# Kernel tuning notes

Hardware: AMD Instinct MI355X
Metric: run time of the kernel (lower is better)

## Reference

```python
import jax, jax.numpy as jnp
import numpy as np

NUM_SKILLS = 50000
HIDDEN = 64
B, T = 8192, 1024
EPS = 1e-6


def setup_inputs() -> dict:
    key = jax.random.key(0)
    ks = jax.random.split(key, 8)
    X = jax.random.randint(ks[0], (B,), 0, NUM_SKILLS)
    y = jax.random.randint(ks[1], (B, T), 0, 2, dtype=jnp.int32)
    embed = jax.random.normal(ks[2], (NUM_SKILLS, HIDDEN), jnp.float32)
    bound = 1.0 / np.sqrt(HIDDEN)
    W0 = jax.random.uniform(ks[3], (HIDDEN, HIDDEN), jnp.float32, -bound, bound)
    b0 = jnp.zeros((HIDDEN,), jnp.float32)
    W1 = jax.random.uniform(ks[4], (HIDDEN, HIDDEN), jnp.float32, -bound, bound)
    b1 = jnp.zeros((HIDDEN,), jnp.float32)
    Wout = jax.random.uniform(ks[5], (HIDDEN, 4), jnp.float32, -bound, bound)
    bout = jnp.zeros((4,), jnp.float32)
    return {"X": X, "y": y, "embed": embed, "W0": W0, "b0": b0,
            "W1": W1, "b1": b1, "Wout": Wout, "bout": bout}


def reference(X, y, embed, W0, b0, W1, b1, Wout, bout):
    # Per-student BKT params from embedding + 2-layer MLP + sigmoid, clamped
    h = embed[X]                                   # (B, H)
    h = jax.nn.relu(h @ W0 + b0)
    h = jax.nn.relu(h @ W1 + b1)
    params = jnp.clip(jax.nn.sigmoid(h @ Wout + bout), EPS, 1.0 - EPS)  # (B, 4)
    l, g, s, prior = params[:, 0], params[:, 1], params[:, 2], params[:, 3]

    def step(latent, y_t):
        true_correct = jnp.where(y_t == -1, 0, y_t)
        correct = latent * (1.0 - s) + (1.0 - latent) * g
        k_t1 = latent * (1.0 - s) / correct
        k_t0 = latent * s / (latent * s + (1.0 - latent) * (1.0 - g))
        k_t = jnp.where(true_correct > 0.5, k_t1, k_t0)
        next_latent = jnp.clip(k_t + (1.0 - k_t) * l, EPS, 1.0 - EPS)
        return next_latent, (correct, latent)

    _, (corrects, latents) = jax.lax.scan(step, prior, y.T)  # scan over T
    return corrects.T, latents.T                            # (B, T) each
```

## Files before the change

### kernel.cpp

```cpp
#include <hip/hip_runtime.h>

#define TSTEPS 1024
#define NROWS  8192
#define CLEN   16
#define KEPS   1e-6f

__device__ __forceinline__ float clampP(float x) {
    return fminf(fmaxf(x, KEPS), 1.f - KEPS);
}
__device__ __forceinline__ float sigm(float v) {
    return 1.0f / (1.0f + __expf(-v));
}

__global__ __launch_bounds__(256) void bkt_params_v4(
    const int* __restrict__ X, const float* __restrict__ embed,
    const float* __restrict__ W0, const float* __restrict__ b0,
    const float* __restrict__ W1, const float* __restrict__ b1,
    const float* __restrict__ Wout, const float* __restrict__ bout,
    float4* __restrict__ params)
{
    const int lane    = threadIdx.x & 63;
    const int wid     = threadIdx.x >> 6;
    const int rowbase = blockIdx.x * 16 + wid * 4;

    __shared__ float sh[4][4][64];
    float (*shw)[64] = sh[wid];

    #pragma unroll
    for (int rs = 0; rs < 4; ++rs) {
        const int skill = X[rowbase + rs];
        shw[rs][lane] = embed[(size_t)skill * 64 + lane];
    }
    __syncthreads();

    float a0 = b0[lane], a1 = a0, a2 = a0, a3 = a0;
    #pragma unroll
    for (int k4 = 0; k4 < 16; ++k4) {
        const float4 e0 = *(const float4*)&shw[0][k4 * 4];
        const float4 e1 = *(const float4*)&shw[1][k4 * 4];
        const float4 e2 = *(const float4*)&shw[2][k4 * 4];
        const float4 e3 = *(const float4*)&shw[3][k4 * 4];
        const float w0 = W0[(k4 * 4 + 0) * 64 + lane];
        const float w1 = W0[(k4 * 4 + 1) * 64 + lane];
        const float w2 = W0[(k4 * 4 + 2) * 64 + lane];
        const float w3 = W0[(k4 * 4 + 3) * 64 + lane];
        a0 = fmaf(e0.x, w0, a0); a0 = fmaf(e0.y, w1, a0); a0 = fmaf(e0.z, w2, a0); a0 = fmaf(e0.w, w3, a0);
        a1 = fmaf(e1.x, w0, a1); a1 = fmaf(e1.y, w1, a1); a1 = fmaf(e1.z, w2, a1); a1 = fmaf(e1.w, w3, a1);
        a2 = fmaf(e2.x, w0, a2); a2 = fmaf(e2.y, w1, a2); a2 = fmaf(e2.z, w2, a2); a2 = fmaf(e2.w, w3, a2);
        a3 = fmaf(e3.x, w0, a3); a3 = fmaf(e3.y, w1, a3); a3 = fmaf(e3.z, w2, a3); a3 = fmaf(e3.w, w3, a3);
    }
    __syncthreads();
    shw[0][lane] = fmaxf(a0, 0.f);
    shw[1][lane] = fmaxf(a1, 0.f);
    shw[2][lane] = fmaxf(a2, 0.f);
    shw[3][lane] = fmaxf(a3, 0.f);
    __syncthreads();

    a0 = b1[lane]; a1 = a0; a2 = a0; a3 = a0;
    #pragma unroll
    for (int k4 = 0; k4 < 16; ++k4) {
        const float4 e0 = *(const float4*)&shw[0][k4 * 4];
        const float4 e1 = *(const float4*)&shw[1][k4 * 4];
        const float4 e2 = *(const float4*)&shw[2][k4 * 4];
        const float4 e3 = *(const float4*)&shw[3][k4 * 4];
        const float w0 = W1[(k4 * 4 + 0) * 64 + lane];
        const float w1 = W1[(k4 * 4 + 1) * 64 + lane];
        const float w2 = W1[(k4 * 4 + 2) * 64 + lane];
        const float w3 = W1[(k4 * 4 + 3) * 64 + lane];
        a0 = fmaf(e0.x, w0, a0); a0 = fmaf(e0.y, w1, a0); a0 = fmaf(e0.z, w2, a0); a0 = fmaf(e0.w, w3, a0);
        a1 = fmaf(e1.x, w0, a1); a1 = fmaf(e1.y, w1, a1); a1 = fmaf(e1.z, w2, a1); a1 = fmaf(e1.w, w3, a1);
        a2 = fmaf(e2.x, w0, a2); a2 = fmaf(e2.y, w1, a2); a2 = fmaf(e2.z, w2, a2); a2 = fmaf(e2.w, w3, a2);
        a3 = fmaf(e3.x, w0, a3); a3 = fmaf(e3.y, w1, a3); a3 = fmaf(e3.z, w2, a3); a3 = fmaf(e3.w, w3, a3);
    }
    const float h0r = fmaxf(a0, 0.f), h1r = fmaxf(a1, 0.f);
    const float h2r = fmaxf(a2, 0.f), h3r = fmaxf(a3, 0.f);

    const float4 wo = ((const float4*)Wout)[lane];
    float p[4][4];
    p[0][0] = h0r * wo.x; p[0][1] = h0r * wo.y; p[0][2] = h0r * wo.z; p[0][3] = h0r * wo.w;
    p[1][0] = h1r * wo.x; p[1][1] = h1r * wo.y; p[1][2] = h1r * wo.z; p[1][3] = h1r * wo.w;
    p[2][0] = h2r * wo.x; p[2][1] = h2r * wo.y; p[2][2] = h2r * wo.z; p[2][3] = h2r * wo.w;
    p[3][0] = h3r * wo.x; p[3][1] = h3r * wo.y; p[3][2] = h3r * wo.z; p[3][3] = h3r * wo.w;
    #pragma unroll
    for (int off = 32; off >= 1; off >>= 1) {
        #pragma unroll
        for (int rs = 0; rs < 4; ++rs)
            #pragma unroll
            for (int c = 0; c < 4; ++c)
                p[rs][c] += __shfl_xor(p[rs][c], off, 64);
    }
    const float4 bo = *(const float4*)bout;
    float v0 = (lane == 0) ? p[0][0] : (lane == 1) ? p[1][0] : (lane == 2) ? p[2][0] : p[3][0];
    float v1 = (lane == 0) ? p[0][1] : (lane == 1) ? p[1][1] : (lane == 2) ? p[2][1] : p[3][1];
    float v2 = (lane == 0) ? p[0][2] : (lane == 1) ? p[1][2] : (lane == 2) ? p[2][2] : p[3][2];
    float v3 = (lane == 0) ? p[0][3] : (lane == 1) ? p[1][3] : (lane == 2) ? p[2][3] : p[3][3];
    if (lane < 4) {
        float4 r;
        r.x = clampP(sigm(v0 + bo.x));
        r.y = clampP(sigm(v1 + bo.y));
        r.z = clampP(sigm(v2 + bo.z));
        r.w = clampP(sigm(v3 + bo.w));
        params[rowbase + lane] = r;
    }
}

__global__ __launch_bounds__(256) void bkt_scan_v5(
    const int* __restrict__ y, const float4* __restrict__ params,
    float* __restrict__ out_corr, float* __restrict__ out_lat)
{
    const int lane = threadIdx.x & 63;
    const int wid  = threadIdx.x >> 6;
    const int row  = blockIdx.x * 4 + wid;

    __shared__ float shbuf[4][2][64 * 17];
    float* shc = shbuf[wid][0];
    float* shl = shbuf[wid][1];

    const float4 p = params[row];
    const float l = p.x, g = p.y, s = p.z, prior = p.w;

    const int4* yrow = (const int4*)(y + (size_t)row * TSTEPS);
    unsigned long long B[4][4];
    #pragma unroll
    for (int j = 0; j < 4; ++j) {
        const int4 v = yrow[j * 64 + lane];
        B[j][0] = __ballot(v.x > 0);
        B[j][1] = __ballot(v.y > 0);
        B[j][2] = __ballot(v.z > 0);
        B[j][3] = __ballot(v.w > 0);
    }
    const int jsel  = lane >> 4;
    const int ibase = (lane & 15) * 4;
    unsigned msk = 0;
    #pragma unroll
    for (int e = 0; e < 4; ++e) {
        const unsigned long long be =
            (jsel == 0) ? B[0][e] : (jsel == 1) ? B[1][e] :
            (jsel == 2) ? B[2][e] : B[3][e];
        const unsigned n  = (unsigned)(be >> ibase) & 0xFu;
        const unsigned sp = (n & 1u) | ((n & 2u) << 3) | ((n & 4u) << 6) | ((n & 8u) << 9);
        msk |= sp << e;
    }

    const float c1 = 1.f - s - g, d1 = g;
    const float e00_1 = fmaf(l, c1, (1.f - l) * (1.f - s));
    const float e01_1 = l * d1;
    const float c0 = s + g - 1.f, d0 = 1.f - g;
    const float e00_0 = fmaf(l, c0, (1.f - l) * s);
    const float e01_0 = l * d0;

    float m00 = 1.f, m01 = 0.f, m10 = 0.f, m11 = 1.f;
    #pragma unroll
    for (int t = 0; t < CLEN; ++t) {
        const bool one = (msk >> t) & 1u;
        const float e00 = one ? e00_1 : e00_0;
        const float e01 = one ? e01_1 : e01_0;
        const float e10 = one ? c1 : c0;
        const float e11 = one ? d1 : d0;
        const float n00 = fmaf(e00, m00, e01 * m10);
        const float n01 = fmaf(e00, m01, e01 * m11);
        const float n10 = fmaf(e10, m00, e11 * m10);
        const float n11 = fmaf(e10, m01, e11 * m11);
        if ((t & 3) == 3) {
            const float inv = __builtin_amdgcn_rcpf(n11);
            m00 = n00 * inv; m01 = n01 * inv; m10 = n10 * inv; m11 = 1.f;
        } else {
            m00 = n00; m01 = n01; m10 = n10; m11 = n11;
        }
    }

    float s00 = m00, s01 = m01, s10 = m10, s11 = m11;
    #pragma unroll
    for (int d = 1; d < 64; d <<= 1) {
        const float t00 = __shfl_up(s00, d, 64);
        const float t01 = __shfl_up(s01, d, 64);
        const float t10 = __shfl_up(s10, d, 64);
        const float t11 = __shfl_up(s11, d, 64);
        if (lane >= d) {
            const float r00 = fmaf(s00, t00, s01 * t10);
            const float r01 = fmaf(s00, t01, s01 * t11);
            const float r10 = fmaf(s10, t00, s11 * t10);
            const float r11 = fmaf(s10, t01, s11 * t11);
            const float inv = __builtin_amdgcn_rcpf(r11);
            s00 = r00 * inv; s01 = r01 * inv; s10 = r10 * inv; s11 = 1.f;
        }
    }
    const float x00 = __shfl_up(s00, 1, 64);
    const float x01 = __shfl_up(s01, 1, 64);
    const float x10 = __shfl_up(s10, 1, 64);
    const float x11 = __shfl_up(s11, 1, 64);
    float L0;
    if (lane == 0) {
        L0 = prior;
    } else {
        const float num = fmaf(x00, prior, x01);
        const float den = fmaf(x10, prior, x11);
        L0 = clampP(num * __builtin_amdgcn_rcpf(den));
    }

    const float a   = 1.f - s;
    const float omg = 1.f - g;
    const float oml = 1.f - l;
    float cr[CLEN], lt[CLEN];
    float Lc = L0;
    #pragma unroll
    for (int t = 0; t < CLEN; ++t) {
        const float correct = fmaf(Lc, c1, g);
        const float den0    = fmaf(Lc, c0, omg);
        const float k1 = (Lc * a) * __builtin_amdgcn_rcpf(correct);
        const float k0 = (Lc * s) * __builtin_amdgcn_rcpf(den0);
        const bool one = (msk >> t) & 1u;
        const float k = one ? k1 : k0;
        cr[t] = correct;
        lt[t] = Lc;
        Lc = clampP(fmaf(k, oml, l));
    }

    #pragma unroll
    for (int t = 0; t < CLEN; ++t) {
        shc[lane * 17 + t] = cr[t];
        shl[lane * 17 + t] = lt[t];
    }
    __syncthreads();

    float* oc = out_corr + (size_t)row * TSTEPS;
    float* ol = out_lat  + (size_t)row * TSTEPS;
    #pragma unroll
    for (int j = 0; j < 4; ++j) {
        const int c    = j * 16 + (lane >> 2);
        const int q    = (lane & 3) * 4;
        const int base = c * 17 + q;
        float4 vc, vl;
        vc.x = shc[base + 0]; vc.y = shc[base + 1]; vc.z = shc[base + 2]; vc.w = shc[base + 3];
        vl.x = shl[base + 0]; vl.y = shl[base + 1]; vl.z = shl[base + 2]; vl.w = shl[base + 3];
        *(float4*)(oc + j * 256 + lane * 4) = vc;
        *(float4*)(ol + j * 256 + lane * 4) = vl;
    }
}

extern "C" void kernel_launch(void* const* d_in, const int* in_sizes, int n_in,
                              void* d_out, int out_size, void* d_ws, size_t ws_size,
                              hipStream_t stream) {
    const int*   X     = (const int*)  d_in[0];
    const int*   y     = (const int*)  d_in[1];
    const float* embed = (const float*)d_in[2];
    const float* W0    = (const float*)d_in[3];
    const float* b0    = (const float*)d_in[4];
    const float* W1    = (const float*)d_in[5];
    const float* b1    = (const float*)d_in[6];
    const float* Wout  = (const float*)d_in[7];
    const float* bout  = (const float*)d_in[8];

    float* out_corr = (float*)d_out;
    float* out_lat  = out_corr + (size_t)NROWS * TSTEPS;
    float4* paramsb = (float4*)d_ws;

    bkt_params_v4<<<NROWS / 16, 256, 0, stream>>>(X, embed, W0, b0, W1, b1, Wout, bout, paramsb);
    bkt_scan_v5 <<<NROWS / 4,  256, 0, stream>>>(y, paramsb, out_corr, out_lat);
}
```

Measured before the change: 123.9 us.

## Halve scan LDS and registers by recomputing chunk recurrence, use nontemporal I/O

The scan kernel now keeps only one 64x17 LDS staging buffer per wave instead of two. It runs the 16-step chunk recurrence twice: the first pass stages and stores the correct probabilities, the second recomputes and stores the latents, so the per-thread cr/lt arrays go away. The per-step k computation selects the numerator and denominator first, so only one reciprocal is needed, and the y loads and output stores become nontemporal. Launch bounds ask for 8 blocks per CU to raise occupancy, at the cost of doing the recurrence arithmetic twice; the __syncthreads was also removed.

```diff
diff --git a/kernel.cpp b/kernel.cpp
--- a/kernel.cpp
+++ b/kernel.cpp
@@ -4,6 +4,9 @@
 #define NROWS  8192
 #define CLEN   16
 #define KEPS   1e-6f
+
+typedef float f32x4 __attribute__((ext_vector_type(4)));
+typedef int   i32x4 __attribute__((ext_vector_type(4)));
 
 __device__ __forceinline__ float clampP(float x) {
     return fminf(fmaxf(x, KEPS), 1.f - KEPS);
@@ -104,7 +107,7 @@
     }
 }
 
-__global__ __launch_bounds__(256) void bkt_scan_v5(
+__global__ __launch_bounds__(256, 8) void bkt_scan_v6(
     const int* __restrict__ y, const float4* __restrict__ params,
     float* __restrict__ out_corr, float* __restrict__ out_lat)
 {
@@ -112,18 +115,17 @@
     const int wid  = threadIdx.x >> 6;
     const int row  = blockIdx.x * 4 + wid;
 
-    __shared__ float shbuf[4][2][64 * 17];
-    float* shc = shbuf[wid][0];
-    float* shl = shbuf[wid][1];
+    __shared__ float shbuf[4][64 * 17];
+    float* shw = shbuf[wid];
 
     const float4 p = params[row];
     const float l = p.x, g = p.y, s = p.z, prior = p.w;
 
-    const int4* yrow = (const int4*)(y + (size_t)row * TSTEPS);
+    const i32x4* yrow = (const i32x4*)(y + (size_t)row * TSTEPS);
     unsigned long long B[4][4];
     #pragma unroll
     for (int j = 0; j < 4; ++j) {
-        const int4 v = yrow[j * 64 + lane];
+        const i32x4 v = __builtin_nontemporal_load(&yrow[j * 64 + lane]);
         B[j][0] = __ballot(v.x > 0);
         B[j][1] = __ballot(v.y > 0);
         B[j][2] = __ballot(v.z > 0);
@@ -201,40 +203,51 @@
     const float a   = 1.f - s;
     const float omg = 1.f - g;
     const float oml = 1.f - l;
-    float cr[CLEN], lt[CLEN];
+    float* oc = out_corr + (size_t)row * TSTEPS;
+    float* ol = out_lat  + (size_t)row * TSTEPS;
+
     float Lc = L0;
     #pragma unroll
     for (int t = 0; t < CLEN; ++t) {
         const float correct = fmaf(Lc, c1, g);
         const float den0    = fmaf(Lc, c0, omg);
-        const float k1 = (Lc * a) * __builtin_amdgcn_rcpf(correct);
-        const float k0 = (Lc * s) * __builtin_amdgcn_rcpf(den0);
+        shw[lane * 17 + t] = correct;
         const bool one = (msk >> t) & 1u;
-        const float k = one ? k1 : k0;
-        cr[t] = correct;
-        lt[t] = Lc;
+        const float den = one ? correct : den0;
+        const float num = Lc * (one ? a : s);
+        const float k   = num * __builtin_amdgcn_rcpf(den);
         Lc = clampP(fmaf(k, oml, l));
     }
-
-    #pragma unroll
-    for (int t = 0; t < CLEN; ++t) {
-        shc[lane * 17 + t] = cr[t];
-        shl[lane * 17 + t] = lt[t];
-    }
-    __syncthreads();
-
-    float* oc = out_corr + (size_t)row * TSTEPS;
-    float* ol = out_lat  + (size_t)row * TSTEPS;
     #pragma unroll
     for (int j = 0; j < 4; ++j) {
         const int c    = j * 16 + (lane >> 2);
         const int q    = (lane & 3) * 4;
         const int base = c * 17 + q;
-        float4 vc, vl;
-        vc.x = shc[base + 0]; vc.y = shc[base + 1]; vc.z = shc[base + 2]; vc.w = shc[base + 3];
-        vl.x = shl[base + 0]; vl.y = shl[base + 1]; vl.z = shl[base + 2]; vl.w = shl[base + 3];
-        *(float4*)(oc + j * 256 + lane * 4) = vc;
-        *(float4*)(ol + j * 256 + lane * 4) = vl;
+        f32x4 vc;
+        vc.x = shw[base + 0]; vc.y = shw[base + 1]; vc.z = shw[base + 2]; vc.w = shw[base + 3];
+        __builtin_nontemporal_store(vc, (f32x4*)(oc + j * 256 + lane * 4));
+    }
+
+    Lc = L0;
+    #pragma unroll
+    for (int t = 0; t < CLEN; ++t) {
+        const float correct = fmaf(Lc, c1, g);
+        const float den0    = fmaf(Lc, c0, omg);
+        shw[lane * 17 + t] = Lc;
+        const bool one = (msk >> t) & 1u;
+        const float den = one ? correct : den0;
+        const float num = Lc * (one ? a : s);
+        const float k   = num * __builtin_amdgcn_rcpf(den);
+        Lc = clampP(fmaf(k, oml, l));
+    }
+    #pragma unroll
+    for (int j = 0; j < 4; ++j) {
+        const int c    = j * 16 + (lane >> 2);
+        const int q    = (lane & 3) * 4;
+        const int base = c * 17 + q;
+        f32x4 vl;
+        vl.x = shw[base + 0]; vl.y = shw[base + 1]; vl.z = shw[base + 2]; vl.w = shw[base + 3];
+        __builtin_nontemporal_store(vl, (f32x4*)(ol + j * 256 + lane * 4));
     }
 }
 
@@ -256,5 +269,5 @@
     float4* paramsb = (float4*)d_ws;
 
     bkt_params_v4<<<NROWS / 16, 256, 0, stream>>>(X, embed, W0, b0, W1, b1, Wout, bout, paramsb);
-    bkt_scan_v5 <<<NROWS / 4,  256, 0, stream>>>(y, paramsb, out_corr, out_lat);
-}
+    bkt_scan_v6 <<<NROWS / 4,  256, 0, stream>>>(y, paramsb, out_corr, out_lat);
+}
```

Measured after the change: 127.0 us. +2.5%, slower.

## Fuse per-row MLP parameter computation into the BKT scan kernel

Applied to the files above, without the earlier changes.

Merges the parameter MLP and the scan into a single kernel where each wave computes its own row's parameters before scanning, removing the intermediate params buffer and a second launch. The y loads are issued before the MLP so their latency overlaps with the matrix math. The scan loop writes directly to shared memory and uses one reciprocal per step instead of two. Block barriers are dropped in favor of wave-local shared buffers. Weight loads are no longer amortized over four rows per wave, and the code now depends on wave-synchronous LDS ordering.

```diff
diff --git a/kernel.cpp b/kernel.cpp
--- a/kernel.cpp
+++ b/kernel.cpp
@@ -12,131 +12,85 @@
     return 1.0f / (1.0f + __expf(-v));
 }
 
-__global__ __launch_bounds__(256) void bkt_params_v4(
-    const int* __restrict__ X, const float* __restrict__ embed,
+__global__ __launch_bounds__(256) void bkt_fused_v7(
+    const int* __restrict__ X, const int* __restrict__ y,
+    const float* __restrict__ embed,
     const float* __restrict__ W0, const float* __restrict__ b0,
     const float* __restrict__ W1, const float* __restrict__ b1,
     const float* __restrict__ Wout, const float* __restrict__ bout,
-    float4* __restrict__ params)
-{
-    const int lane    = threadIdx.x & 63;
-    const int wid     = threadIdx.x >> 6;
-    const int rowbase = blockIdx.x * 16 + wid * 4;
-
-    __shared__ float sh[4][4][64];
-    float (*shw)[64] = sh[wid];
-
-    #pragma unroll
-    for (int rs = 0; rs < 4; ++rs) {
-        const int skill = X[rowbase + rs];
-        shw[rs][lane] = embed[(size_t)skill * 64 + lane];
-    }
-    __syncthreads();
-
-    float a0 = b0[lane], a1 = a0, a2 = a0, a3 = a0;
-    #pragma unroll
-    for (int k4 = 0; k4 < 16; ++k4) {
-        const float4 e0 = *(const float4*)&shw[0][k4 * 4];
-        const float4 e1 = *(const float4*)&shw[1][k4 * 4];
-        const float4 e2 = *(const float4*)&shw[2][k4 * 4];
-        const float4 e3 = *(const float4*)&shw[3][k4 * 4];
-        const float w0 = W0[(k4 * 4 + 0) * 64 + lane];
-        const float w1 = W0[(k4 * 4 + 1) * 64 + lane];
-        const float w2 = W0[(k4 * 4 + 2) * 64 + lane];
-        const float w3 = W0[(k4 * 4 + 3) * 64 + lane];
-        a0 = fmaf(e0.x, w0, a0); a0 = fmaf(e0.y, w1, a0); a0 = fmaf(e0.z, w2, a0); a0 = fmaf(e0.w, w3, a0);
-        a1 = fmaf(e1.x, w0, a1); a1 = fmaf(e1.y, w1, a1); a1 = fmaf(e1.z, w2, a1); a1 = fmaf(e1.w, w3, a1);
-        a2 = fmaf(e2.x, w0, a2); a2 = fmaf(e2.y, w1, a2); a2 = fmaf(e2.z, w2, a2); a2 = fmaf(e2.w, w3, a2);
-        a3 = fmaf(e3.x, w0, a3); a3 = fmaf(e3.y, w1, a3); a3 = fmaf(e3.z, w2, a3); a3 = fmaf(e3.w, w3, a3);
-    }
-    __syncthreads();
-    shw[0][lane] = fmaxf(a0, 0.f);
-    shw[1][lane] = fmaxf(a1, 0.f);
-    shw[2][lane] = fmaxf(a2, 0.f);
-    shw[3][lane] = fmaxf(a3, 0.f);
-    __syncthreads();
-
-    a0 = b1[lane]; a1 = a0; a2 = a0; a3 = a0;
-    #pragma unroll
-    for (int k4 = 0; k4 < 16; ++k4) {
-        const float4 e0 = *(const float4*)&shw[0][k4 * 4];
-        const float4 e1 = *(const float4*)&shw[1][k4 * 4];
-        const float4 e2 = *(const float4*)&shw[2][k4 * 4];
-        const float4 e3 = *(const float4*)&shw[3][k4 * 4];
-        const float w0 = W1[(k4 * 4 + 0) * 64 + lane];
-        const float w1 = W1[(k4 * 4 + 1) * 64 + lane];
-        const float w2 = W1[(k4 * 4 + 2) * 64 + lane];
-        const float w3 = W1[(k4 * 4 + 3) * 64 + lane];
-        a0 = fmaf(e0.x, w0, a0); a0 = fmaf(e0.y, w1, a0); a0 = fmaf(e0.z, w2, a0); a0 = fmaf(e0.w, w3, a0);
-        a1 = fmaf(e1.x, w0, a1); a1 = fmaf(e1.y, w1, a1); a1 = fmaf(e1.z, w2, a1); a1 = fmaf(e1.w, w3, a1);
-        a2 = fmaf(e2.x, w0, a2); a2 = fmaf(e2.y, w1, a2); a2 = fmaf(e2.z, w2, a2); a2 = fmaf(e2.w, w3, a2);
-        a3 = fmaf(e3.x, w0, a3); a3 = fmaf(e3.y, w1, a3); a3 = fmaf(e3.z, w2, a3); a3 = fmaf(e3.w, w3, a3);
-    }
-    const float h0r = fmaxf(a0, 0.f), h1r = fmaxf(a1, 0.f);
-    const float h2r = fmaxf(a2, 0.f), h3r = fmaxf(a3, 0.f);
-
-    const float4 wo = ((const float4*)Wout)[lane];
-    float p[4][4];
-    p[0][0] = h0r * wo.x; p[0][1] = h0r * wo.y; p[0][2] = h0r * wo.z; p[0][3] = h0r * wo.w;
-    p[1][0] = h1r * wo.x; p[1][1] = h1r * wo.y; p[1][2] = h1r * wo.z; p[1][3] = h1r * wo.w;
-    p[2][0] = h2r * wo.x; p[2][1] = h2r * wo.y; p[2][2] = h2r * wo.z; p[2][3] = h2r * wo.w;
-    p[3][0] = h3r * wo.x; p[3][1] = h3r * wo.y; p[3][2] = h3r * wo.z; p[3][3] = h3r * wo.w;
-    #pragma unroll
-    for (int off = 32; off >= 1; off >>= 1) {
-        #pragma unroll
-        for (int rs = 0; rs < 4; ++rs)
-            #pragma unroll
-            for (int c = 0; c < 4; ++c)
-                p[rs][c] += __shfl_xor(p[rs][c], off, 64);
-    }
-    const float4 bo = *(const float4*)bout;
-    float v0 = (lane == 0) ? p[0][0] : (lane == 1) ? p[1][0] : (lane == 2) ? p[2][0] : p[3][0];
-    float v1 = (lane == 0) ? p[0][1] : (lane == 1) ? p[1][1] : (lane == 2) ? p[2][1] : p[3][1];
-    float v2 = (lane == 0) ? p[0][2] : (lane == 1) ? p[1][2] : (lane == 2) ? p[2][2] : p[3][2];
-    float v3 = (lane == 0) ? p[0][3] : (lane == 1) ? p[1][3] : (lane == 2) ? p[2][3] : p[3][3];
-    if (lane < 4) {
-        float4 r;
-        r.x = clampP(sigm(v0 + bo.x));
-        r.y = clampP(sigm(v1 + bo.y));
-        r.z = clampP(sigm(v2 + bo.z));
-        r.w = clampP(sigm(v3 + bo.w));
-        params[rowbase + lane] = r;
-    }
-}
-
-__global__ __launch_bounds__(256) void bkt_scan_v5(
-    const int* __restrict__ y, const float4* __restrict__ params,
     float* __restrict__ out_corr, float* __restrict__ out_lat)
 {
     const int lane = threadIdx.x & 63;
     const int wid  = threadIdx.x >> 6;
     const int row  = blockIdx.x * 4 + wid;
 
-    __shared__ float shbuf[4][2][64 * 17];
-    float* shc = shbuf[wid][0];
-    float* shl = shbuf[wid][1];
-
-    const float4 p = params[row];
-    const float l = p.x, g = p.y, s = p.z, prior = p.w;
+    __shared__ float hstage[4][64];
+    __shared__ float trbuf[4][2][64 * 17];
+    float* hbuf = hstage[wid];
+    float* shc  = trbuf[wid][0];
+    float* shl  = trbuf[wid][1];
 
     const int4* yrow = (const int4*)(y + (size_t)row * TSTEPS);
-    unsigned long long B[4][4];
-    #pragma unroll
-    for (int j = 0; j < 4; ++j) {
-        const int4 v = yrow[j * 64 + lane];
-        B[j][0] = __ballot(v.x > 0);
-        B[j][1] = __ballot(v.y > 0);
-        B[j][2] = __ballot(v.z > 0);
-        B[j][3] = __ballot(v.w > 0);
-    }
+    const int4 vy0 = yrow[0 * 64 + lane];
+    const int4 vy1 = yrow[1 * 64 + lane];
+    const int4 vy2 = yrow[2 * 64 + lane];
+    const int4 vy3 = yrow[3 * 64 + lane];
+
+    const int skill = X[row];
+    hbuf[lane] = embed[(size_t)skill * 64 + lane];
+    float acc = b0[lane];
+    #pragma unroll
+    for (int k4 = 0; k4 < 16; ++k4) {
+        const float4 e = *(const float4*)&hbuf[k4 * 4];
+        acc = fmaf(e.x, W0[(k4 * 4 + 0) * 64 + lane], acc);
+        acc = fmaf(e.y, W0[(k4 * 4 + 1) * 64 + lane], acc);
+        acc = fmaf(e.z, W0[(k4 * 4 + 2) * 64 + lane], acc);
+        acc = fmaf(e.w, W0[(k4 * 4 + 3) * 64 + lane], acc);
+    }
+    hbuf[lane] = fmaxf(acc, 0.f);
+    acc = b1[lane];
+    #pragma unroll
+    for (int k4 = 0; k4 < 16; ++k4) {
+        const float4 e = *(const float4*)&hbuf[k4 * 4];
+        acc = fmaf(e.x, W1[(k4 * 4 + 0) * 64 + lane], acc);
+        acc = fmaf(e.y, W1[(k4 * 4 + 1) * 64 + lane], acc);
+        acc = fmaf(e.z, W1[(k4 * 4 + 2) * 64 + lane], acc);
+        acc = fmaf(e.w, W1[(k4 * 4 + 3) * 64 + lane], acc);
+    }
+    const float h2 = fmaxf(acc, 0.f);
+
+    const float4 wo = ((const float4*)Wout)[lane];
+    float p0 = h2 * wo.x, p1 = h2 * wo.y, p2 = h2 * wo.z, p3 = h2 * wo.w;
+    #pragma unroll
+    for (int off = 32; off >= 1; off >>= 1) {
+        p0 += __shfl_xor(p0, off, 64);
+        p1 += __shfl_xor(p1, off, 64);
+        p2 += __shfl_xor(p2, off, 64);
+        p3 += __shfl_xor(p3, off, 64);
+    }
+    const float4 bo = *(const float4*)bout;
+    const float l     = clampP(sigm(p0 + bo.x));
+    const float g     = clampP(sigm(p1 + bo.y));
+    const float s     = clampP(sigm(p2 + bo.z));
+    const float prior = clampP(sigm(p3 + bo.w));
+
+    unsigned long long B_[4][4];
+    B_[0][0] = __ballot(vy0.x > 0); B_[0][1] = __ballot(vy0.y > 0);
+    B_[0][2] = __ballot(vy0.z > 0); B_[0][3] = __ballot(vy0.w > 0);
+    B_[1][0] = __ballot(vy1.x > 0); B_[1][1] = __ballot(vy1.y > 0);
+    B_[1][2] = __ballot(vy1.z > 0); B_[1][3] = __ballot(vy1.w > 0);
+    B_[2][0] = __ballot(vy2.x > 0); B_[2][1] = __ballot(vy2.y > 0);
+    B_[2][2] = __ballot(vy2.z > 0); B_[2][3] = __ballot(vy2.w > 0);
+    B_[3][0] = __ballot(vy3.x > 0); B_[3][1] = __ballot(vy3.y > 0);
+    B_[3][2] = __ballot(vy3.z > 0); B_[3][3] = __ballot(vy3.w > 0);
     const int jsel  = lane >> 4;
     const int ibase = (lane & 15) * 4;
     unsigned msk = 0;
     #pragma unroll
     for (int e = 0; e < 4; ++e) {
         const unsigned long long be =
-            (jsel == 0) ? B[0][e] : (jsel == 1) ? B[1][e] :
-            (jsel == 2) ? B[2][e] : B[3][e];
+            (jsel == 0) ? B_[0][e] : (jsel == 1) ? B_[1][e] :
+            (jsel == 2) ? B_[2][e] : B_[3][e];
         const unsigned n  = (unsigned)(be >> ibase) & 0xFu;
         const unsigned sp = (n & 1u) | ((n & 2u) << 3) | ((n & 4u) << 6) | ((n & 8u) << 9);
         msk |= sp << e;
@@ -201,27 +155,19 @@
     const float a   = 1.f - s;
     const float omg = 1.f - g;
     const float oml = 1.f - l;
-    float cr[CLEN], lt[CLEN];
     float Lc = L0;
     #pragma unroll
     for (int t = 0; t < CLEN; ++t) {
         const float correct = fmaf(Lc, c1, g);
         const float den0    = fmaf(Lc, c0, omg);
-        const float k1 = (Lc * a) * __builtin_amdgcn_rcpf(correct);
-        const float k0 = (Lc * s) * __builtin_amdgcn_rcpf(den0);
+        shc[lane * 17 + t] = correct;
+        shl[lane * 17 + t] = Lc;
         const bool one = (msk >> t) & 1u;
-        const float k = one ? k1 : k0;
-        cr[t] = correct;
-        lt[t] = Lc;
+        const float den = one ? correct : den0;
+        const float num = Lc * (one ? a : s);
+        const float k   = num * __builtin_amdgcn_rcpf(den);
         Lc = clampP(fmaf(k, oml, l));
     }
-
-    #pragma unroll
-    for (int t = 0; t < CLEN; ++t) {
-        shc[lane * 17 + t] = cr[t];
-        shl[lane * 17 + t] = lt[t];
-    }
-    __syncthreads();
 
     float* oc = out_corr + (size_t)row * TSTEPS;
     float* ol = out_lat  + (size_t)row * TSTEPS;
@@ -253,8 +199,7 @@
 
     float* out_corr = (float*)d_out;
     float* out_lat  = out_corr + (size_t)NROWS * TSTEPS;
-    float4* paramsb = (float4*)d_ws;
-
-    bkt_params_v4<<<NROWS / 16, 256, 0, stream>>>(X, embed, W0, b0, W1, b1, Wout, bout, paramsb);
-    bkt_scan_v5 <<<NROWS / 4,  256, 0, stream>>>(y, paramsb, out_corr, out_lat);
-}
+
+    bkt_fused_v7<<<NROWS / 4, 256, 0, stream>>>(
+        X, y, embed, W0, b0, W1, b1, Wout, bout, out_corr, out_lat);
+}
```

Result: no change. 121.7 us (-1.7%).
